# Kernel optimization log

Measured on AMD Instinct MI355X. Metric: run time of the kernel, lower is better.

Reference implementation:

```python
import jax, jax.numpy as jnp
import numpy as np

B, S, H = 16, 2048, 1024

def setup_inputs() -> dict:
    key = jax.random.key(0)
    k1, k2, k3, k4 = jax.random.split(key, 4)
    x = jax.random.normal(k1, (B, S, H), dtype=jnp.float32)
    # nn.Linear weights, stored as (out, in); y = x @ W.T
    scale = 1.0 / np.sqrt(H)
    W_q = jax.random.uniform(k2, (H, H), jnp.float32, -scale, scale)
    W_k = jax.random.uniform(k3, (H, H), jnp.float32, -scale, scale)
    W_v = jax.random.uniform(k4, (H, H), jnp.float32, -scale, scale)
    return {"x": x, "W_q": W_q, "W_k": W_k, "W_v": W_v}

def reference(x, W_q, W_k, W_v):
    # x: (B,S,H); W_*: (H,H) torch Linear layout (out,in)
    Q = jnp.einsum('bsh,oh->bso', x, W_q)
    K = jnp.einsum('bsh,oh->bso', x, W_k)
    V = jnp.einsum('bsh,oh->bso', x, W_v)
    scale = jnp.asarray(x.shape[-1] ** 0.5, dtype=x.dtype)
    energy = jnp.einsum('bqd,bkd->bqk', Q, K) / scale      # (B,S,S)
    attn = jax.nn.softmax(energy, axis=-1)                  # (B,S,S)
    attended = jnp.einsum('bqk,bkd->bqd', attn, V)          # (B,S,H)
    context = attended.mean(axis=1)                         # (B,H)
    attn_weights = attn.mean(axis=1)                        # (B,S)
    return (context, attn_weights)
```

## Files before the change

### kernel.cpp

```cpp
#include <hip/hip_runtime.h>
#include <hip/hip_bf16.h>
#include <stdint.h>

#define BB 16
#define SS 2048
#define HH 1024

using bf16 = __hip_bfloat16;
typedef __attribute__((ext_vector_type(8))) short short8;
typedef __attribute__((ext_vector_type(4))) float f32x4;

typedef unsigned int __attribute__((address_space(1))) as1_uint;
typedef unsigned int __attribute__((address_space(3))) as3_uint;

static constexpr size_t WS_XB   = 0;
static constexpr size_t WS_G    = 67108864;
static constexpr size_t WS_P    = 134217728;
static constexpr size_t WS_WQT  = 134217728;
static constexpr size_t WS_WKT  = 136314880;
static constexpr size_t WS_MT   = 138412032;
static constexpr size_t WS_LSUM = 201326592;
static constexpr size_t WS_T    = 201457664;
static constexpr size_t WS_NEED = 201523200;

__device__ __forceinline__ void async_copy16(bf16* lds_dst, const bf16* gsrc) {
    __builtin_amdgcn_global_load_lds((const as1_uint*)gsrc, (as3_uint*)lds_dst, 16, 0, 0);
}

__device__ __forceinline__ unsigned char f32_to_e4m3(float x) {
#if __has_builtin(__builtin_amdgcn_cvt_pk_fp8_f32)
    return (unsigned char)(__builtin_amdgcn_cvt_pk_fp8_f32(x, x, 0, false) & 0xff);
#else
    if (x >= 0.015625f) {
        union { float f; unsigned u; } v; v.f = x;
        int e = (v.u >> 23) & 0xff;
        unsigned m = v.u & 0x7fffff;
        unsigned mant = m >> 20;
        unsigned rem = m & 0xfffff;
        mant += (rem > 0x80000u) || (rem == 0x80000u && (mant & 1));
        int oe = e - 120;
        if (mant == 8) { mant = 0; oe += 1; }
        return (unsigned char)((oe << 3) | mant);
    }
    int code = (int)rintf(x * 512.0f);
    return (unsigned char)code;
#endif
}

__device__ __forceinline__ float e4m3_to_f32(unsigned char b) {
#if __has_builtin(__builtin_amdgcn_cvt_pk_f32_fp8)
    auto v = __builtin_amdgcn_cvt_pk_f32_fp8((int)b, false);
    return v[0];
#else
    int e = (b >> 3) & 15, m = b & 7;
    if (e) { union { unsigned u; float f; } v; v.u = ((unsigned)(e + 120) << 23) | ((unsigned)m << 20); return v.f; }
    return (float)m * 0.001953125f;
#endif
}

__global__ __launch_bounds__(256) void cast_x_kernel(const float* __restrict__ x,
                                                     bf16* __restrict__ xb, int n4) {
    int stride = gridDim.x * blockDim.x;
    for (int i = blockIdx.x * blockDim.x + threadIdx.x; i < n4; i += stride) {
        float4 v = reinterpret_cast<const float4*>(x)[i];
        union { bf16 h[4]; uint2 u; } p;
        p.h[0] = __float2bfloat16(v.x); p.h[1] = __float2bfloat16(v.y);
        p.h[2] = __float2bfloat16(v.z); p.h[3] = __float2bfloat16(v.w);
        reinterpret_cast<uint2*>(xb)[i] = p.u;
    }
}

__global__ __launch_bounds__(256) void transpose_w_kernel(const float* __restrict__ wq,
                                                          const float* __restrict__ wk,
                                                          bf16* __restrict__ wqT,
                                                          bf16* __restrict__ wkT) {
    __shared__ float tile[64][65];
    const float* src = blockIdx.z ? wk : wq;
    bf16* dst = blockIdx.z ? wkT : wqT;
    const int o0 = blockIdx.y * 64, i0 = blockIdx.x * 64;
    const int tr = threadIdx.x >> 4;
    const int tc = (threadIdx.x & 15) * 4;
#pragma unroll
    for (int k = 0; k < 4; ++k) {
        float4 v = *reinterpret_cast<const float4*>(src + (size_t)(o0 + tr + k * 16) * 1024 + i0 + tc);
        tile[tr + k * 16][tc + 0] = v.x; tile[tr + k * 16][tc + 1] = v.y;
        tile[tr + k * 16][tc + 2] = v.z; tile[tr + k * 16][tc + 3] = v.w;
    }
    __syncthreads();
#pragma unroll
    for (int k = 0; k < 4; ++k) {
        int ri = tr + k * 16;
        union { bf16 h[4]; uint2 u; } p;
#pragma unroll
        for (int j = 0; j < 4; ++j) p.h[j] = __float2bfloat16(tile[tc + j][ri]);
        *reinterpret_cast<uint2*>(dst + (size_t)(i0 + ri) * 1024 + o0 + tc) = p.u;
    }
}

__device__ __forceinline__ void mfma_mainloop(const bf16* __restrict__ Abase, int lda,
                                              const bf16* __restrict__ Bbase, int ldb,
                                              int K, bf16* As, bf16* Bs, f32x4 acc[4][4]) {
    const int tid = threadIdx.x;
    const int wid = tid >> 6, lane = tid & 63;
    const int wm = wid >> 1, wn = wid & 1;
    const int srow = lane >> 3;
    const int scol = (lane & 7) * 8;
    for (int kt = 0; kt < K; kt += 64) {
#pragma unroll
        for (int i = 0; i < 4; ++i) {
            int blkrow = (wid * 4 + i) * 8;
            async_copy16(As + blkrow * 64, Abase + (size_t)(blkrow + srow) * lda + kt + scol);
            async_copy16(Bs + blkrow * 64, Bbase + (size_t)(blkrow + srow) * ldb + kt + scol);
        }
        __syncthreads();
#pragma unroll
        for (int kk = 0; kk < 2; ++kk) {
            short8 a[4], b[4];
#pragma unroll
            for (int m = 0; m < 4; ++m)
                a[m] = *reinterpret_cast<const short8*>(
                    As + (wm * 64 + m * 16 + (lane & 15)) * 64 + kk * 32 + (lane >> 4) * 8);
#pragma unroll
            for (int n = 0; n < 4; ++n)
                b[n] = *reinterpret_cast<const short8*>(
                    Bs + (wn * 64 + n * 16 + (lane & 15)) * 64 + kk * 32 + (lane >> 4) * 8);
#pragma unroll
            for (int m = 0; m < 4; ++m)
#pragma unroll
                for (int n = 0; n < 4; ++n)
                    acc[m][n] = __builtin_amdgcn_mfma_f32_16x16x32_bf16(a[m], b[n], acc[m][n], 0, 0, 0);
        }
        __syncthreads();
    }
}

__global__ __launch_bounds__(256) void gemm_mt(const bf16* __restrict__ wkT,
                                               const bf16* __restrict__ wqT,
                                               bf16* __restrict__ Mt) {
    __shared__ bf16 As[128 * 64], Bs[128 * 64];
    f32x4 acc[4][4];
#pragma unroll
    for (int m = 0; m < 4; ++m)
#pragma unroll
        for (int n = 0; n < 4; ++n) { acc[m][n][0]=0.f; acc[m][n][1]=0.f; acc[m][n][2]=0.f; acc[m][n][3]=0.f; }
    const int bx = blockIdx.x, by = blockIdx.y;
    mfma_mainloop(wkT + (size_t)by * 128 * 1024, 1024,
                  wqT + (size_t)bx * 128 * 1024, 1024, 1024, As, Bs, acc);
    const int lane = threadIdx.x & 63, wid = threadIdx.x >> 6;
    const int wm = wid >> 1, wn = wid & 1;
    const int row0 = by * 128 + wm * 64 + ((lane >> 4) << 2);
    const int col0 = bx * 128 + wn * 64 + (lane & 15);
#pragma unroll
    for (int m = 0; m < 4; ++m)
#pragma unroll
        for (int n = 0; n < 4; ++n)
#pragma unroll
            for (int r = 0; r < 4; ++r)
                Mt[(size_t)(row0 + m * 16 + r) * 1024 + col0 + n * 16] =
                    __float2bfloat16(acc[m][n][r] * 0.03125f);
}

static constexpr int NT256 = 16;

__device__ __forceinline__ void stage_A256(char* As_base, int qm,
                                           const bf16* __restrict__ Ag, int kt) {
    const int tid = threadIdx.x;
    const int wid = tid >> 6;
#pragma unroll
    for (int i = 0; i < 2; ++i) {
        int beta = (i * 512 + tid) * 16;
        int rho  = beta >> 7;
        int c    = beta & 127;
        int cs   = c ^ ((rho & 7) << 4);
        int wm_r = rho >> 6, j = rho & 63;
        int grow = wm_r * 128 + qm * 64 + j;
        const bf16* src = Ag + (size_t)grow * 1024 + kt * 64 + (cs >> 1);
        char* dst = As_base + qm * 16384 + i * 8192 + wid * 1024;
        async_copy16((bf16*)dst, src);
    }
}

__device__ __forceinline__ void stage_B256(char* Bs_base, int qn,
                                           const bf16* __restrict__ Bg, int kt) {
    const int tid = threadIdx.x;
    const int wid = tid >> 6;
#pragma unroll
    for (int i = 0; i < 2; ++i) {
        int beta = (i * 512 + tid) * 16;
        int rho  = beta >> 7;
        int c    = beta & 127;
        int cs   = c ^ ((rho & 7) << 4);
        int wn_r = rho >> 5, s = rho & 31;
        int grow = wn_r * 64 + qn * 32 + s;
        const bf16* src = Bg + (size_t)grow * 1024 + kt * 64 + (cs >> 1);
        char* dst = Bs_base + qn * 16384 + i * 8192 + wid * 1024;
        async_copy16((bf16*)dst, src);
    }
}

__device__ __forceinline__ void gemm256_mainloop(const bf16* __restrict__ Ag,
                                                 const bf16* __restrict__ Bg,
                                                 char* lds, f32x4 acc[8][4]) {
    const int tid = threadIdx.x;
    const int lane = tid & 63;
    const int wm = (tid >> 6) >> 2;
    const int wn = (tid >> 6) & 3;

#pragma unroll
    for (int m = 0; m < 8; ++m)
#pragma unroll
        for (int n = 0; n < 4; ++n) { acc[m][n][0]=0.f; acc[m][n][1]=0.f; acc[m][n][2]=0.f; acc[m][n][3]=0.f; }

    char* A0 = lds;            char* B0 = lds + 32768;
    char* A1 = lds + 65536;    char* B1 = lds + 98304;

    stage_A256(A0, 0, Ag, 0);
    stage_A256(A0, 1, Ag, 0);
    stage_B256(B0, 0, Bg, 0);
    stage_B256(B0, 1, Bg, 0);
    stage_A256(A1, 0, Ag, 1);
    stage_B256(B1, 0, Bg, 1);
    asm volatile("s_waitcnt vmcnt(4)" ::: "memory");
    __builtin_amdgcn_s_barrier();

#pragma unroll 1
    for (int t = 0; t < NT256; ++t) {
        char* As  = (t & 1) ? A1 : A0;
        char* Bs  = (t & 1) ? B1 : B0;
        char* Aso = (t & 1) ? A0 : A1;
        char* Bso = (t & 1) ? B0 : B1;
#pragma unroll
        for (int ph = 0; ph < 4; ++ph) {
            const int qm = ph >> 1, qn = ph & 1;
            short8 a[4][2], b[2][2];
#pragma unroll
            for (int mi = 0; mi < 4; ++mi)
#pragma unroll
                for (int kk = 0; kk < 2; ++kk) {
                    int row = qm * 128 + wm * 64 + mi * 16 + (lane & 15);
                    int col = kk * 64 + (lane >> 4) * 16;
                    int off = (row * 128 + col) ^ ((row & 7) << 4);
                    a[mi][kk] = *reinterpret_cast<const short8*>(As + off);
                }
#pragma unroll
            for (int ni = 0; ni < 2; ++ni)
#pragma unroll
                for (int kk = 0; kk < 2; ++kk) {
                    int row = qn * 128 + wn * 32 + ni * 16 + (lane & 15);
                    int col = kk * 64 + (lane >> 4) * 16;
                    int off = (row * 128 + col) ^ ((row & 7) << 4);
                    b[ni][kk] = *reinterpret_cast<const short8*>(Bs + off);
                }
            if (ph == 0)      { if (t + 1 < NT256) stage_B256(Bso, 1, Bg, t + 1); }
            else if (ph == 1) { if (t + 1 < NT256) stage_A256(Aso, 1, Ag, t + 1); }
            else if (ph == 2) { if (t + 2 < NT256) stage_A256(As,  0, Ag, t + 2); }
            else              { if (t + 2 < NT256) stage_B256(Bs,  0, Bg, t + 2); }
            __builtin_amdgcn_s_barrier();
            __builtin_amdgcn_s_setprio(1);
#pragma unroll
            for (int mi = 0; mi < 4; ++mi)
#pragma unroll
                for (int ni = 0; ni < 2; ++ni)
#pragma unroll
                    for (int kk = 0; kk < 2; ++kk)
                        acc[qm * 4 + mi][qn * 2 + ni] =
                            __builtin_amdgcn_mfma_f32_16x16x32_bf16(
                                a[mi][kk], b[ni][kk], acc[qm * 4 + mi][qn * 2 + ni], 0, 0, 0);
            __builtin_amdgcn_s_setprio(0);
            asm volatile("s_waitcnt lgkmcnt(0)" ::: "memory");
            __builtin_amdgcn_s_barrier();
        }
        if (t + 2 < NT256) asm volatile("s_waitcnt vmcnt(4)" ::: "memory");
        else               asm volatile("s_waitcnt vmcnt(0)" ::: "memory");
        __builtin_amdgcn_s_barrier();
    }
}

__global__ __launch_bounds__(512, 2) void gemm_g256(const bf16* __restrict__ xb,
                                                    const bf16* __restrict__ Mt,
                                                    bf16* __restrict__ G) {
    extern __shared__ char lds[];
    f32x4 acc[8][4];
    const int bx = blockIdx.x, by = blockIdx.y;
    gemm256_mainloop(xb + (size_t)by * 256 * 1024, Mt + (size_t)bx * 256 * 1024, lds, acc);
    const int lane = threadIdx.x & 63, wid = threadIdx.x >> 6;
    const int wm = wid >> 2, wn = wid & 3;
    const int row0 = by * 256 + wm * 128 + ((lane >> 4) << 2);
    const int col0 = bx * 256 + wn * 64 + (lane & 15);
#pragma unroll
    for (int mi = 0; mi < 8; ++mi)
#pragma unroll
        for (int ni = 0; ni < 4; ++ni)
#pragma unroll
            for (int r = 0; r < 4; ++r)
                G[(size_t)(row0 + mi * 16 + r) * 1024 + col0 + ni * 16] =
                    __float2bfloat16(acc[mi][ni][r]);
}

__global__ __launch_bounds__(512, 2) void energy_fused256(const bf16* __restrict__ G,
                                                          const bf16* __restrict__ xb,
                                                          unsigned char* __restrict__ P,
                                                          float* __restrict__ lsum) {
    extern __shared__ char lds[];
    f32x4 acc[8][4];
    const int bx = blockIdx.x, by = blockIdx.y, bz = blockIdx.z;
    gemm256_mainloop(G + (size_t)(bz * 2048 + by * 256) * 1024,
                     xb + (size_t)(bz * 2048 + bx * 256) * 1024, lds, acc);
    const int lane = threadIdx.x & 63, wid = threadIdx.x >> 6;
    const int wm = wid >> 2, wn = wid & 3;
    const int q0 = bz * 2048 + by * 256 + wm * 128 + ((lane >> 4) << 2);
    const int k0 = bx * 256 + wn * 64 + (lane & 15);
#pragma unroll
    for (int mi = 0; mi < 8; ++mi) {
        float s[4] = {0.f, 0.f, 0.f, 0.f};
#pragma unroll
        for (int ni = 0; ni < 4; ++ni)
#pragma unroll
            for (int r = 0; r < 4; ++r) {
                float e = __expf(acc[mi][ni][r]);
                unsigned char c = f32_to_e4m3(e);
                P[(size_t)(q0 + mi * 16 + r) * 2048 + k0 + ni * 16] = c;
                s[r] += e4m3_to_f32(c);
            }
#pragma unroll
        for (int off = 1; off < 16; off <<= 1)
#pragma unroll
            for (int r = 0; r < 4; ++r) s[r] += __shfl_xor(s[r], off, 64);
        if ((lane & 15) == 0) {
#pragma unroll
            for (int r = 0; r < 4; ++r) atomicAdd(&lsum[q0 + mi * 16 + r], s[r]);
        }
    }
}

__global__ __launch_bounds__(256) void colsum_kernel(const unsigned char* __restrict__ P,
                                                     const float* __restrict__ lsum,
                                                     float* __restrict__ aw) {
    const int b = blockIdx.y, qc = blockIdx.x, t = threadIdx.x;
    float acc[8] = {0.f, 0.f, 0.f, 0.f, 0.f, 0.f, 0.f, 0.f};
    const unsigned char* base = P + (size_t)(b * 2048 + qc * 128) * 2048 + t * 8;
    const float* ls = lsum + b * 2048 + qc * 128;
    for (int q = 0; q < 128; ++q) {
        float w = 1.0f / ls[q];
        uint2 v = *reinterpret_cast<const uint2*>(base + (size_t)q * 2048);
#if __has_builtin(__builtin_amdgcn_cvt_pk_f32_fp8)
        auto p0 = __builtin_amdgcn_cvt_pk_f32_fp8((int)v.x, false);
        auto p1 = __builtin_amdgcn_cvt_pk_f32_fp8((int)v.x, true);
        auto p2 = __builtin_amdgcn_cvt_pk_f32_fp8((int)v.y, false);
        auto p3 = __builtin_amdgcn_cvt_pk_f32_fp8((int)v.y, true);
        acc[0] += p0[0] * w; acc[1] += p0[1] * w;
        acc[2] += p1[0] * w; acc[3] += p1[1] * w;
        acc[4] += p2[0] * w; acc[5] += p2[1] * w;
        acc[6] += p3[0] * w; acc[7] += p3[1] * w;
#else
        unsigned char by8[8];
        *reinterpret_cast<uint2*>(by8) = v;
#pragma unroll
        for (int j = 0; j < 8; ++j) acc[j] += e4m3_to_f32(by8[j]) * w;
#endif
    }
#pragma unroll
    for (int j = 0; j < 8; ++j)
        atomicAdd(&aw[b * 2048 + t * 8 + j], acc[j] * (1.0f / 2048.0f));
}

__global__ __launch_bounds__(256) void av_x_kernel(const float* __restrict__ aw,
                                                   const float* __restrict__ x,
                                                   float* __restrict__ t) {
    const int b = blockIdx.y;
    const int kc = blockIdx.x;
    const int tid = threadIdx.x;
    float4 acc = {0.f, 0.f, 0.f, 0.f};
    const int k0 = kc * 128;
#pragma unroll 4
    for (int k = k0; k < k0 + 128; ++k) {
        float w = aw[b * 2048 + k];
        float4 xv = *reinterpret_cast<const float4*>(x + (size_t)(b * 2048 + k) * 1024 + tid * 4);
        acc.x += w * xv.x; acc.y += w * xv.y; acc.z += w * xv.z; acc.w += w * xv.w;
    }
    float* tp = t + b * 1024 + tid * 4;
    atomicAdd(tp + 0, acc.x); atomicAdd(tp + 1, acc.y);
    atomicAdd(tp + 2, acc.z); atomicAdd(tp + 3, acc.w);
}

__global__ __launch_bounds__(256) void ctx_gemv_kernel(const float* __restrict__ t,
                                                       const float* __restrict__ wv,
                                                       float* __restrict__ ctx) {
    const int b = blockIdx.y;
    const int wid = threadIdx.x >> 6, lane = threadIdx.x & 63;
    const int o = blockIdx.x * 4 + wid;
    const float4* t4 = reinterpret_cast<const float4*>(t + b * 1024);
    const float4* w4 = reinterpret_cast<const float4*>(wv + (size_t)o * 1024);
    float s = 0.f;
#pragma unroll
    for (int j = lane; j < 256; j += 64) {
        float4 a = t4[j], w = w4[j];
        s += a.x * w.x + a.y * w.y + a.z * w.z + a.w * w.w;
    }
#pragma unroll
    for (int off = 1; off < 64; off <<= 1) s += __shfl_xor(s, off, 64);
    if (lane == 0) ctx[b * 1024 + o] = s;
}

__global__ void ws_too_small_kernel(float* out) {
    if (threadIdx.x == 0 && blockIdx.x == 0) out[0] = 12345.0f;
}

extern "C" void kernel_launch(void* const* d_in, const int* in_sizes, int n_in,
                              void* d_out, int out_size, void* d_ws, size_t ws_size,
                              hipStream_t stream) {
    const float* x  = (const float*)d_in[0];
    const float* wq = (const float*)d_in[1];
    const float* wk = (const float*)d_in[2];
    const float* wv = (const float*)d_in[3];
    float* out = (float*)d_out;
    float* ctx = out;
    float* aw  = out + 16384;

    if (ws_size < WS_NEED) {
        hipMemsetAsync(d_out, 0, (size_t)out_size * sizeof(float), stream);
        ws_too_small_kernel<<<1, 64, 0, stream>>>(out);
        return;
    }

    char* ws = (char*)d_ws;
    bf16* xb   = (bf16*)(ws + WS_XB);
    bf16* G    = (bf16*)(ws + WS_G);
    unsigned char* P = (unsigned char*)(ws + WS_P);
    bf16* wqT  = (bf16*)(ws + WS_WQT);
    bf16* wkT  = (bf16*)(ws + WS_WKT);
    bf16* Mt   = (bf16*)(ws + WS_MT);
    float* lsum = (float*)(ws + WS_LSUM);
    float* t    = (float*)(ws + WS_T);

    hipMemsetAsync(d_out, 0, (size_t)out_size * sizeof(float), stream);
    hipMemsetAsync(lsum, 0, 131072 + 65536, stream);

    cast_x_kernel<<<2048, 256, 0, stream>>>(x, xb, (BB * SS * HH) / 4);
    transpose_w_kernel<<<dim3(16, 16, 2), 256, 0, stream>>>(wq, wk, wqT, wkT);

    gemm_mt<<<dim3(8, 8), 256, 0, stream>>>(wkT, wqT, Mt);
    gemm_g256<<<dim3(4, 128), 512, 131072, stream>>>(xb, Mt, G);

    energy_fused256<<<dim3(8, 8, 16), 512, 131072, stream>>>(G, xb, P, lsum);
    colsum_kernel<<<dim3(16, 16), 256, 0, stream>>>(P, lsum, aw);

    av_x_kernel<<<dim3(16, 16), 256, 0, stream>>>(aw, x, t);
    ctx_gemv_kernel<<<dim3(256, 16), 256, 0, stream>>>(t, wv, ctx);
}
```

Baseline: 368.4 us.

## Shrink Mt GEMM tiles, reuse fragments across phases in 256 GEMM, read bf16 x in av

Replaces the 128x128 Mt GEMM with a 64x64 tile version launched on a 16x16 grid, giving 256 blocks instead of 64 to fill more CUs. The 256-tile mainloop is reordered so A and B fragments are kept in registers across quadrant phases, cutting redundant LDS reads, and the prologue staging order is changed. av_x_kernel now reads the bf16 copy of x instead of fp32, halving its memory traffic at some precision cost.

Measured after the change: 324.4 us. 1.14x faster.

```diff
diff --git a/kernel.cpp b/kernel.cpp
--- a/kernel.cpp
+++ b/kernel.cpp
@@ -25,6 +25,10 @@
 
 __device__ __forceinline__ void async_copy16(bf16* lds_dst, const bf16* gsrc) {
     __builtin_amdgcn_global_load_lds((const as1_uint*)gsrc, (as3_uint*)lds_dst, 16, 0, 0);
+}
+
+__device__ __forceinline__ float bf2f(unsigned short u) {
+    union { unsigned i; float f; } v; v.i = (unsigned)u << 16; return v.f;
 }
 
 __device__ __forceinline__ unsigned char f32_to_e4m3(float x) {
@@ -97,63 +101,53 @@
     }
 }
 
-__device__ __forceinline__ void mfma_mainloop(const bf16* __restrict__ Abase, int lda,
-                                              const bf16* __restrict__ Bbase, int ldb,
-                                              int K, bf16* As, bf16* Bs, f32x4 acc[4][4]) {
-    const int tid = threadIdx.x;
-    const int wid = tid >> 6, lane = tid & 63;
+__global__ __launch_bounds__(256) void gemm_mt64(const bf16* __restrict__ wkT,
+                                                 const bf16* __restrict__ wqT,
+                                                 bf16* __restrict__ Mt) {
+    __shared__ bf16 As[64 * 64], Bs[64 * 64];
+    f32x4 acc[2][2];
+#pragma unroll
+    for (int m = 0; m < 2; ++m)
+#pragma unroll
+        for (int n = 0; n < 2; ++n) { acc[m][n][0]=0.f; acc[m][n][1]=0.f; acc[m][n][2]=0.f; acc[m][n][3]=0.f; }
+    const int tid = threadIdx.x, wid = tid >> 6, lane = tid & 63;
     const int wm = wid >> 1, wn = wid & 1;
-    const int srow = lane >> 3;
-    const int scol = (lane & 7) * 8;
-    for (int kt = 0; kt < K; kt += 64) {
-#pragma unroll
-        for (int i = 0; i < 4; ++i) {
-            int blkrow = (wid * 4 + i) * 8;
-            async_copy16(As + blkrow * 64, Abase + (size_t)(blkrow + srow) * lda + kt + scol);
-            async_copy16(Bs + blkrow * 64, Bbase + (size_t)(blkrow + srow) * ldb + kt + scol);
+    const int srow = lane >> 3, scol = (lane & 7) * 8;
+    const bf16* Ab = wkT + (size_t)blockIdx.y * 64 * 1024;
+    const bf16* Bb = wqT + (size_t)blockIdx.x * 64 * 1024;
+    for (int kt = 0; kt < 1024; kt += 64) {
+#pragma unroll
+        for (int i = 0; i < 2; ++i) {
+            int row0 = i * 32 + wid * 8;
+            async_copy16(As + row0 * 64, Ab + (size_t)(row0 + srow) * 1024 + kt + scol);
+            async_copy16(Bs + row0 * 64, Bb + (size_t)(row0 + srow) * 1024 + kt + scol);
         }
         __syncthreads();
 #pragma unroll
         for (int kk = 0; kk < 2; ++kk) {
-            short8 a[4], b[4];
-#pragma unroll
-            for (int m = 0; m < 4; ++m)
+            short8 a[2], b[2];
+#pragma unroll
+            for (int m = 0; m < 2; ++m)
                 a[m] = *reinterpret_cast<const short8*>(
-                    As + (wm * 64 + m * 16 + (lane & 15)) * 64 + kk * 32 + (lane >> 4) * 8);
-#pragma unroll
-            for (int n = 0; n < 4; ++n)
+                    As + (wm * 32 + m * 16 + (lane & 15)) * 64 + kk * 32 + (lane >> 4) * 8);
+#pragma unroll
+            for (int n = 0; n < 2; ++n)
                 b[n] = *reinterpret_cast<const short8*>(
-                    Bs + (wn * 64 + n * 16 + (lane & 15)) * 64 + kk * 32 + (lane >> 4) * 8);
-#pragma unroll
-            for (int m = 0; m < 4; ++m)
-#pragma unroll
-                for (int n = 0; n < 4; ++n)
+                    Bs + (wn * 32 + n * 16 + (lane & 15)) * 64 + kk * 32 + (lane >> 4) * 8);
+#pragma unroll
+            for (int m = 0; m < 2; ++m)
+#pragma unroll
+                for (int n = 0; n < 2; ++n)
                     acc[m][n] = __builtin_amdgcn_mfma_f32_16x16x32_bf16(a[m], b[n], acc[m][n], 0, 0, 0);
         }
         __syncthreads();
     }
-}
-
-__global__ __launch_bounds__(256) void gemm_mt(const bf16* __restrict__ wkT,
-                                               const bf16* __restrict__ wqT,
-                                               bf16* __restrict__ Mt) {
-    __shared__ bf16 As[128 * 64], Bs[128 * 64];
-    f32x4 acc[4][4];
-#pragma unroll
-    for (int m = 0; m < 4; ++m)
-#pragma unroll
-        for (int n = 0; n < 4; ++n) { acc[m][n][0]=0.f; acc[m][n][1]=0.f; acc[m][n][2]=0.f; acc[m][n][3]=0.f; }
-    const int bx = blockIdx.x, by = blockIdx.y;
-    mfma_mainloop(wkT + (size_t)by * 128 * 1024, 1024,
-                  wqT + (size_t)bx * 128 * 1024, 1024, 1024, As, Bs, acc);
-    const int lane = threadIdx.x & 63, wid = threadIdx.x >> 6;
-    const int wm = wid >> 1, wn = wid & 1;
-    const int row0 = by * 128 + wm * 64 + ((lane >> 4) << 2);
-    const int col0 = bx * 128 + wn * 64 + (lane & 15);
-#pragma unroll
-    for (int m = 0; m < 4; ++m)
-#pragma unroll
-        for (int n = 0; n < 4; ++n)
+    const int row0 = blockIdx.y * 64 + wm * 32 + ((lane >> 4) << 2);
+    const int col0 = blockIdx.x * 64 + wn * 32 + (lane & 15);
+#pragma unroll
+    for (int m = 0; m < 2; ++m)
+#pragma unroll
+        for (int n = 0; n < 2; ++n)
 #pragma unroll
             for (int r = 0; r < 4; ++r)
                 Mt[(size_t)(row0 + m * 16 + r) * 1024 + col0 + n * 16] =
@@ -215,13 +209,15 @@
     char* A1 = lds + 65536;    char* B1 = lds + 98304;
 
     stage_A256(A0, 0, Ag, 0);
-    stage_A256(A0, 1, Ag, 0);
     stage_B256(B0, 0, Bg, 0);
     stage_B256(B0, 1, Bg, 0);
+    stage_A256(A0, 1, Ag, 0);
     stage_A256(A1, 0, Ag, 1);
     stage_B256(B1, 0, Bg, 1);
     asm volatile("s_waitcnt vmcnt(4)" ::: "memory");
     __builtin_amdgcn_s_barrier();
+
+    short8 a[4][2], b0[2][2], b1[2][2];
 
 #pragma unroll 1
     for (int t = 0; t < NT256; ++t) {
@@ -229,47 +225,96 @@
         char* Bs  = (t & 1) ? B1 : B0;
         char* Aso = (t & 1) ? A0 : A1;
         char* Bso = (t & 1) ? B0 : B1;
-#pragma unroll
-        for (int ph = 0; ph < 4; ++ph) {
-            const int qm = ph >> 1, qn = ph & 1;
-            short8 a[4][2], b[2][2];
-#pragma unroll
-            for (int mi = 0; mi < 4; ++mi)
-#pragma unroll
-                for (int kk = 0; kk < 2; ++kk) {
-                    int row = qm * 128 + wm * 64 + mi * 16 + (lane & 15);
-                    int col = kk * 64 + (lane >> 4) * 16;
-                    int off = (row * 128 + col) ^ ((row & 7) << 4);
-                    a[mi][kk] = *reinterpret_cast<const short8*>(As + off);
-                }
+
+#pragma unroll
+        for (int mi = 0; mi < 4; ++mi)
+#pragma unroll
+            for (int kk = 0; kk < 2; ++kk) {
+                int row = wm * 64 + mi * 16 + (lane & 15);
+                int off = (row * 128 + kk * 64 + (lane >> 4) * 16) ^ ((row & 7) << 4);
+                a[mi][kk] = *reinterpret_cast<const short8*>(As + off);
+            }
+#pragma unroll
+        for (int ni = 0; ni < 2; ++ni)
+#pragma unroll
+            for (int kk = 0; kk < 2; ++kk) {
+                int row = wn * 32 + ni * 16 + (lane & 15);
+                int off = (row * 128 + kk * 64 + (lane >> 4) * 16) ^ ((row & 7) << 4);
+                b0[ni][kk] = *reinterpret_cast<const short8*>(Bs + off);
+            }
+        if (t + 1 < NT256) stage_B256(Bso, 1, Bg, t + 1);
+        __builtin_amdgcn_s_barrier();
+        asm volatile("s_waitcnt lgkmcnt(0)" ::: "memory");
+        __builtin_amdgcn_s_setprio(1);
+#pragma unroll
+        for (int mi = 0; mi < 4; ++mi)
 #pragma unroll
             for (int ni = 0; ni < 2; ++ni)
 #pragma unroll
-                for (int kk = 0; kk < 2; ++kk) {
-                    int row = qn * 128 + wn * 32 + ni * 16 + (lane & 15);
-                    int col = kk * 64 + (lane >> 4) * 16;
-                    int off = (row * 128 + col) ^ ((row & 7) << 4);
-                    b[ni][kk] = *reinterpret_cast<const short8*>(Bs + off);
-                }
-            if (ph == 0)      { if (t + 1 < NT256) stage_B256(Bso, 1, Bg, t + 1); }
-            else if (ph == 1) { if (t + 1 < NT256) stage_A256(Aso, 1, Ag, t + 1); }
-            else if (ph == 2) { if (t + 2 < NT256) stage_A256(As,  0, Ag, t + 2); }
-            else              { if (t + 2 < NT256) stage_B256(Bs,  0, Bg, t + 2); }
-            __builtin_amdgcn_s_barrier();
-            __builtin_amdgcn_s_setprio(1);
-#pragma unroll
-            for (int mi = 0; mi < 4; ++mi)
-#pragma unroll
-                for (int ni = 0; ni < 2; ++ni)
-#pragma unroll
-                    for (int kk = 0; kk < 2; ++kk)
-                        acc[qm * 4 + mi][qn * 2 + ni] =
-                            __builtin_amdgcn_mfma_f32_16x16x32_bf16(
-                                a[mi][kk], b[ni][kk], acc[qm * 4 + mi][qn * 2 + ni], 0, 0, 0);
-            __builtin_amdgcn_s_setprio(0);
-            asm volatile("s_waitcnt lgkmcnt(0)" ::: "memory");
-            __builtin_amdgcn_s_barrier();
-        }
+                for (int kk = 0; kk < 2; ++kk)
+                    acc[mi][ni] = __builtin_amdgcn_mfma_f32_16x16x32_bf16(
+                        a[mi][kk], b0[ni][kk], acc[mi][ni], 0, 0, 0);
+        __builtin_amdgcn_s_setprio(0);
+        __builtin_amdgcn_s_barrier();
+
+#pragma unroll
+        for (int ni = 0; ni < 2; ++ni)
+#pragma unroll
+            for (int kk = 0; kk < 2; ++kk) {
+                int row = 128 + wn * 32 + ni * 16 + (lane & 15);
+                int off = (row * 128 + kk * 64 + (lane >> 4) * 16) ^ ((row & 7) << 4);
+                b1[ni][kk] = *reinterpret_cast<const short8*>(Bs + off);
+            }
+        if (t + 1 < NT256) stage_A256(Aso, 1, Ag, t + 1);
+        __builtin_amdgcn_s_barrier();
+        asm volatile("s_waitcnt lgkmcnt(0)" ::: "memory");
+        __builtin_amdgcn_s_setprio(1);
+#pragma unroll
+        for (int mi = 0; mi < 4; ++mi)
+#pragma unroll
+            for (int ni = 0; ni < 2; ++ni)
+#pragma unroll
+                for (int kk = 0; kk < 2; ++kk)
+                    acc[mi][2 + ni] = __builtin_amdgcn_mfma_f32_16x16x32_bf16(
+                        a[mi][kk], b1[ni][kk], acc[mi][2 + ni], 0, 0, 0);
+        __builtin_amdgcn_s_setprio(0);
+        __builtin_amdgcn_s_barrier();
+
+#pragma unroll
+        for (int mi = 0; mi < 4; ++mi)
+#pragma unroll
+            for (int kk = 0; kk < 2; ++kk) {
+                int row = 128 + wm * 64 + mi * 16 + (lane & 15);
+                int off = (row * 128 + kk * 64 + (lane >> 4) * 16) ^ ((row & 7) << 4);
+                a[mi][kk] = *reinterpret_cast<const short8*>(As + off);
+            }
+        if (t + 2 < NT256) stage_A256(As, 0, Ag, t + 2);
+        __builtin_amdgcn_s_barrier();
+        asm volatile("s_waitcnt lgkmcnt(0)" ::: "memory");
+        __builtin_amdgcn_s_setprio(1);
+#pragma unroll
+        for (int mi = 0; mi < 4; ++mi)
+#pragma unroll
+            for (int ni = 0; ni < 2; ++ni)
+#pragma unroll
+                for (int kk = 0; kk < 2; ++kk)
+                    acc[4 + mi][2 + ni] = __builtin_amdgcn_mfma_f32_16x16x32_bf16(
+                        a[mi][kk], b1[ni][kk], acc[4 + mi][2 + ni], 0, 0, 0);
+        __builtin_amdgcn_s_setprio(0);
+        __builtin_amdgcn_s_barrier();
+
+        if (t + 2 < NT256) stage_B256(Bs, 0, Bg, t + 2);
+        __builtin_amdgcn_s_barrier();
+        __builtin_amdgcn_s_setprio(1);
+#pragma unroll
+        for (int mi = 0; mi < 4; ++mi)
+#pragma unroll
+            for (int ni = 0; ni < 2; ++ni)
+#pragma unroll
+                for (int kk = 0; kk < 2; ++kk)
+                    acc[4 + mi][ni] = __builtin_amdgcn_mfma_f32_16x16x32_bf16(
+                        a[mi][kk], b0[ni][kk], acc[4 + mi][ni], 0, 0, 0);
+        __builtin_amdgcn_s_setprio(0);
         if (t + 2 < NT256) asm volatile("s_waitcnt vmcnt(4)" ::: "memory");
         else               asm volatile("s_waitcnt vmcnt(0)" ::: "memory");
         __builtin_amdgcn_s_barrier();
@@ -365,7 +410,7 @@
 }
 
 __global__ __launch_bounds__(256) void av_x_kernel(const float* __restrict__ aw,
-                                                   const float* __restrict__ x,
+                                                   const bf16* __restrict__ xb,
                                                    float* __restrict__ t) {
     const int b = blockIdx.y;
     const int kc = blockIdx.x;
@@ -375,8 +420,11 @@
 #pragma unroll 4
     for (int k = k0; k < k0 + 128; ++k) {
         float w = aw[b * 2048 + k];
-        float4 xv = *reinterpret_cast<const float4*>(x + (size_t)(b * 2048 + k) * 1024 + tid * 4);
-        acc.x += w * xv.x; acc.y += w * xv.y; acc.z += w * xv.z; acc.w += w * xv.w;
+        uint2 v = *reinterpret_cast<const uint2*>(xb + (size_t)(b * 2048 + k) * 1024 + tid * 4);
+        acc.x += w * bf2f((unsigned short)(v.x & 0xffff));
+        acc.y += w * bf2f((unsigned short)(v.x >> 16));
+        acc.z += w * bf2f((unsigned short)(v.y & 0xffff));
+        acc.w += w * bf2f((unsigned short)(v.y >> 16));
     }
     float* tp = t + b * 1024 + tid * 4;
     atomicAdd(tp + 0, acc.x); atomicAdd(tp + 1, acc.y);
@@ -439,12 +487,12 @@
     cast_x_kernel<<<2048, 256, 0, stream>>>(x, xb, (BB * SS * HH) / 4);
     transpose_w_kernel<<<dim3(16, 16, 2), 256, 0, stream>>>(wq, wk, wqT, wkT);
 
-    gemm_mt<<<dim3(8, 8), 256, 0, stream>>>(wkT, wqT, Mt);
+    gemm_mt64<<<dim3(16, 16), 256, 0, stream>>>(wkT, wqT, Mt);
     gemm_g256<<<dim3(4, 128), 512, 131072, stream>>>(xb, Mt, G);
 
     energy_fused256<<<dim3(8, 8, 16), 512, 131072, stream>>>(G, xb, P, lsum);
     colsum_kernel<<<dim3(16, 16), 256, 0, stream>>>(P, lsum, aw);
 
-    av_x_kernel<<<dim3(16, 16), 256, 0, stream>>>(aw, x, t);
+    av_x_kernel<<<dim3(16, 16), 256, 0, stream>>>(aw, xb, t);
     ctx_gemv_kernel<<<dim3(256, 16), 256, 0, stream>>>(t, wv, ctx);
 }
```
